# Performance work log

Hardware: AMD Instinct MI355X
Metric: run time of the kernel (lower is better)

The kernel has to match this reference:

```python
import jax, jax.numpy as jnp
import numpy as np
from jax import lax

FH, FW = 5, 5            # kernel_size
DIL_Y, DIL_X = 2, 2      # kernel_dilation
GROUPS = 2               # num_deform_groups
STRIDE_Y, STRIDE_X = 1, 1
PAD_Y, PAD_X = FH // 2, FW // 2
DPAD_Y, DPAD_X = DIL_Y * PAD_Y, DIL_X * PAD_X
OFFSET_NUM = FH * FW * GROUPS * 2  # 100


def setup_inputs() -> dict:
    key = jax.random.key(0)
    k1, k2 = jax.random.split(key, 2)
    B, H, W, C = 2, 192, 384, 16
    volume = jax.random.uniform(k1, (B, H, W, C), dtype=jnp.float32)
    # flax nn.Conv defaults: lecun_normal kernel, zeros bias
    w_off = jax.random.normal(k2, (FH, FW, C, OFFSET_NUM), dtype=jnp.float32) / np.sqrt(FH * FW * C)
    b_off = jnp.zeros((OFFSET_NUM,), dtype=jnp.float32)
    return {"volume": volume, "w_off": w_off, "b_off": b_off}


def _forward(volume, w_off, b_off):
    B, H, W, C = volume.shape
    # offset-predicting conv (VALID, dilated)
    off = lax.conv_general_dilated(
        volume, w_off, (STRIDE_Y, STRIDE_X), 'VALID',
        rhs_dilation=(DIL_Y, DIL_X),
        dimension_numbers=('NHWC', 'HWIO', 'NHWC')) + b_off
    oh, ow = off.shape[1], off.shape[2]
    off = off.reshape(B, oh, ow, FH * FW, 2, GROUPS)
    dy, dx = off[..., 0, :], off[..., 1, :]  # (B,oh,ow,K,G)
    kys = jnp.arange(-DPAD_Y, DPAD_Y + 1, DIL_Y, dtype=jnp.float32)  # (FH,)
    kxs = jnp.arange(-DPAD_X, DPAD_X + 1, DIL_X, dtype=jnp.float32)  # (FW,)
    kv = jnp.repeat(kys, FW)[None, None, None, :, None]  # flat kernel grid, y-offsets
    ku = jnp.tile(kxs, FH)[None, None, None, :, None]    # flat kernel grid, x-offsets
    # Faithful to the source code (including its quirks): rx = kernel_y + dy and
    # ry = kernel_x + dx (names/axes swapped in the original _pixel), the base
    # pixel coordinate is NOT added to the sampling position, and w1 uses the
    # base row index y instead of ry.
    rx = kv + dy
    ry = ku + dx
    x0 = rx.astype(jnp.int32); x1 = x0 + 1  # int32 cast truncates toward zero, as in source
    y0 = ry.astype(jnp.int32); y1 = y0 + 1
    y0 = jnp.clip(y0, 0, H - 1); y1 = jnp.clip(y1, 0, H - 1)
    x0 = jnp.clip(x0, 0, W - 1); x1 = jnp.clip(x1, 0, W - 1)
    by = jnp.arange(DPAD_Y, H - DPAD_Y, STRIDE_Y, dtype=jnp.float32)[None, :, None, None, None]
    w0 = (y1 - ry) * (x1 - rx)
    w1 = (y1 - by) * (rx - x0)
    w2 = (ry - y0) * (x1 - rx)
    w3 = (ry - y0) * (rx - x0)
    # The original sums w_i * p_i over the 4 taps AND all C channels; since the
    # bilinear weights are channel-independent this equals gathering from the
    # channel-summed volume (same math, far fewer gathered bytes).
    S = volume.sum(-1)  # (B,H,W)
    gather = jax.vmap(lambda s, yi, xi: s[yi, xi])  # per-batch fancy gather
    out = (w0 * gather(S, y0, x0) + w1 * gather(S, y0, x1)
           + w2 * gather(S, y1, x0) + w3 * gather(S, y1, x1))  # (B,oh,ow,K,G)
    out = out.reshape(B, oh, ow, FH, FW, GROUPS)
    return jnp.transpose(out, (0, 5, 1, 2, 3, 4))  # (B,G,oh,ow,FH,FW)


def reference(volume, w_off, b_off):
    return _forward(volume, w_off, b_off)
```

## Files before the change

### kernel.cpp

```cpp
#include <hip/hip_runtime.h>

#define HH 192
#define WW 384
#define CC 16
#define OH 184
#define OW 376
#define NTAP 25
#define TILE 64

__global__ void prep_kernel(const float* __restrict__ vol, float* __restrict__ S,
                            const float* __restrict__ w_off, float4* __restrict__ w_t,
                            int nS, int nW) {
    int idx = blockIdx.x * 256 + threadIdx.x;
    if (idx < nS) {
        const float4* p = reinterpret_cast<const float4*>(vol + (size_t)idx * CC);
        float4 a = p[0], b = p[1], c = p[2], d = p[3];
        S[idx] = ((a.x + a.y) + (a.z + a.w)) + ((b.x + b.y) + (b.z + b.w))
               + ((c.x + c.y) + (c.z + c.w)) + ((d.x + d.y) + (d.z + d.w));
    }
    if (idx < nW) {
        int kk = (idx >> 4) % 25;
        int tn = idx / (25 * 16);
        w_t[idx] = *reinterpret_cast<const float4*>(w_off + ((idx & 15) + kk * 16) * 100 + 4 * tn);
    }
}

#define DOT4Q(acc, v, w0, w1, w2, w3) do {                                   \
    acc.x = fmaf(v.x, w0.x, acc.x); acc.x = fmaf(v.y, w1.x, acc.x);          \
    acc.x = fmaf(v.z, w2.x, acc.x); acc.x = fmaf(v.w, w3.x, acc.x);          \
    acc.y = fmaf(v.x, w0.y, acc.y); acc.y = fmaf(v.y, w1.y, acc.y);          \
    acc.y = fmaf(v.z, w2.y, acc.y); acc.y = fmaf(v.w, w3.y, acc.y);          \
    acc.z = fmaf(v.x, w0.z, acc.z); acc.z = fmaf(v.y, w1.z, acc.z);          \
    acc.z = fmaf(v.z, w2.z, acc.z); acc.z = fmaf(v.w, w3.z, acc.z);          \
    acc.w = fmaf(v.x, w0.w, acc.w); acc.w = fmaf(v.y, w1.w, acc.w);          \
    acc.w = fmaf(v.z, w2.w, acc.w); acc.w = fmaf(v.w, w3.w, acc.w);          \
} while (0)

__global__ __launch_bounds__(320) void dconv_kernel(
    const float* __restrict__ vol, const float* __restrict__ w_t,
    const float* __restrict__ b_off, const float* __restrict__ S,
    float* __restrict__ out)
{
    __shared__ float4 lds[4][8][73];

    const int tid  = threadIdx.x;
    const int lane = tid & 63;
    const int wid  = tid >> 6;
    const int z    = blockIdx.z;
    const int kg   = z % 5;
    const int rem  = z / 5;
    const int p    = rem & 1;
    const int b    = rem >> 1;
    const int gy   = blockIdx.y;
    const int ox0  = blockIdx.x * TILE;
    const int tn   = __builtin_amdgcn_readfirstlane(kg * 5 + wid);

    {
        const float* __restrict__ vb = vol + (size_t)((b * HH + p + 8 * gy) * WW) * CC;
        if (tid < 288) {
            const int q    = tid & 3;
            const int colr = tid >> 2;
            int colg = ox0 + colr; if (colg > WW - 1) colg = WW - 1;
            const float* src = vb + (size_t)colg * CC + 4 * q;
            #pragma unroll
            for (int t = 0; t < 8; ++t)
                lds[q][t][colr] = *reinterpret_cast<const float4*>(src + (size_t)(2 * t) * WW * CC);
        }
    }
    __syncthreads();

    const float4* __restrict__ wt = reinterpret_cast<const float4*>(w_t) + tn * (25 * 16);
    const float4 bo = *reinterpret_cast<const float4*>(b_off + 4 * tn);
    float4 acc0 = bo, acc1 = bo, acc2 = bo, acc3 = bo;

    #pragma unroll 1
    for (int r = 0; r < 5; ++r) {
        #pragma unroll
        for (int kx = 0; kx < 5; ++kx) {
            const float4* __restrict__ W = wt + (r * 5 + kx) * 16;
            const int cl = lane + 2 * kx;
            #pragma unroll
            for (int cq = 0; cq < 4; ++cq) {
                const float4 w0 = W[4 * cq + 0], w1 = W[4 * cq + 1];
                const float4 w2 = W[4 * cq + 2], w3 = W[4 * cq + 3];
                const float4 v0 = lds[cq][r + 0][cl];
                const float4 v1 = lds[cq][r + 1][cl];
                const float4 v2 = lds[cq][r + 2][cl];
                const float4 v3 = lds[cq][r + 3][cl];
                DOT4Q(acc0, v0, w0, w1, w2, w3);
                DOT4Q(acc1, v1, w0, w1, w2, w3);
                DOT4Q(acc2, v2, w0, w1, w2, w3);
                DOT4Q(acc3, v3, w0, w1, w2, w3);
            }
        }
    }

    const int ox = ox0 + lane;
    if (ox < OW) {
        const int kyt = tn / 5, kxt = tn % 5;
        const float kv = (float)(2 * kyt - 4);
        const float ku = (float)(2 * kxt - 4);
        const float* __restrict__ Sb = S + b * HH * WW;
        #pragma unroll
        for (int j = 0; j < 4; ++j) {
            const int oy = p + 8 * gy + 2 * j;
            const float4 acc = j == 0 ? acc0 : j == 1 ? acc1 : j == 2 ? acc2 : acc3;
            const float byv = (float)(4 + oy);
            #pragma unroll
            for (int g = 0; g < 2; ++g) {
                const float dy = g == 0 ? acc.x : acc.y;
                const float dx = g == 0 ? acc.z : acc.w;
                const float rx = kv + dy;
                const float ry = ku + dx;
                int x0 = (int)rx;
                int x1 = x0 + 1;
                int y0 = (int)ry;
                int y1 = y0 + 1;
                int x0c = min(max(x0, 0), WW - 1);
                int x1c = min(max(x1, 0), WW - 1);
                int y0c = min(max(y0, 0), HH - 1);
                int y1c = min(max(y1, 0), HH - 1);
                const float fx0 = (float)x0c, fx1 = (float)x1c;
                const float fy0 = (float)y0c, fy1 = (float)y1c;
                const float w0v = (fy1 - ry)  * (fx1 - rx);
                const float w1v = (fy1 - byv) * (rx - fx0);
                const float w2v = (ry - fy0)  * (fx1 - rx);
                const float w3v = (ry - fy0)  * (rx - fx0);
                const float s00 = Sb[y0c * WW + x0c];
                const float s01 = Sb[y0c * WW + x1c];
                const float s10 = Sb[y1c * WW + x0c];
                const float s11 = Sb[y1c * WW + x1c];
                out[(size_t)(((b * 2 + g) * OH + oy) * OW + ox) * NTAP + tn]
                    = w0v * s00 + w1v * s01 + w2v * s10 + w3v * s11;
            }
        }
    }
}

extern "C" void kernel_launch(void* const* d_in, const int* in_sizes, int n_in,
                              void* d_out, int out_size, void* d_ws, size_t ws_size,
                              hipStream_t stream) {
    const float* vol   = (const float*)d_in[0];
    const float* w_off = (const float*)d_in[1];
    const float* b_off = (const float*)d_in[2];
    float* out = (float*)d_out;

    float* S   = (float*)d_ws;
    float* w_t = (float*)((char*)d_ws + 2 * HH * WW * 4);

    const int nS = 2 * HH * WW;
    const int nW = NTAP * 25 * 16;
    prep_kernel<<<(nS + 255) / 256, 256, 0, stream>>>(vol, S, w_off, (float4*)w_t, nS, nW);

    dim3 grid((OW + TILE - 1) / TILE, 23, 2 * 2 * 5);
    dconv_kernel<<<grid, 320, 0, stream>>>(vol, w_t, b_off, S, out);
}
```

Measured before the change: 222.5 us.

## Give each wave five taps over two rows instead of one tap over four rows

The work split changes so that each wave computes 5 output taps (one kernel row) for 2 output rows, instead of 1 tap for 4 rows. The grid drops the tap-group dimension and doubles the row-block dimension. Each block loads 6 input rows instead of 8, and the whole grid reads the input volume once per row block rather than five times, cutting LDS fill and global traffic. In exchange each thread keeps 10 float4 accumulators and reads 5 separate weight streams, which raises register pressure and scalar or vector weight loads.

```diff
diff --git a/kernel.cpp b/kernel.cpp
--- a/kernel.cpp
+++ b/kernel.cpp
@@ -41,97 +41,106 @@
     const float* __restrict__ b_off, const float* __restrict__ S,
     float* __restrict__ out)
 {
-    __shared__ float4 lds[4][8][73];
+    __shared__ float4 lds[4][6][73];
 
     const int tid  = threadIdx.x;
     const int lane = tid & 63;
     const int wid  = tid >> 6;
     const int z    = blockIdx.z;
-    const int kg   = z % 5;
-    const int rem  = z / 5;
-    const int p    = rem & 1;
-    const int b    = rem >> 1;
+    const int p    = z & 1;
+    const int b    = z >> 1;
     const int gy   = blockIdx.y;
+    const int oy0  = p + 4 * gy;
     const int ox0  = blockIdx.x * TILE;
-    const int tn   = __builtin_amdgcn_readfirstlane(kg * 5 + wid);
 
     {
-        const float* __restrict__ vb = vol + (size_t)((b * HH + p + 8 * gy) * WW) * CC;
-        if (tid < 288) {
-            const int q    = tid & 3;
-            const int colr = tid >> 2;
+        const float* __restrict__ vb = vol + (size_t)((b * HH + oy0) * WW) * CC;
+        for (int i = tid; i < 6 * 72 * 4; i += 320) {
+            const int colr = i % 72;
+            const int rem  = i / 72;
+            const int t    = rem % 6;
+            const int q    = rem / 6;
             int colg = ox0 + colr; if (colg > WW - 1) colg = WW - 1;
-            const float* src = vb + (size_t)colg * CC + 4 * q;
-            #pragma unroll
-            for (int t = 0; t < 8; ++t)
-                lds[q][t][colr] = *reinterpret_cast<const float4*>(src + (size_t)(2 * t) * WW * CC);
+            lds[q][t][colr] = *reinterpret_cast<const float4*>(
+                vb + (size_t)(2 * t * WW + colg) * CC + 4 * q);
         }
     }
     __syncthreads();
 
-    const float4* __restrict__ wt = reinterpret_cast<const float4*>(w_t) + tn * (25 * 16);
-    const float4 bo = *reinterpret_cast<const float4*>(b_off + 4 * tn);
-    float4 acc0 = bo, acc1 = bo, acc2 = bo, acc3 = bo;
+    const float4* __restrict__ w4 = reinterpret_cast<const float4*>(w_t);
+    const float4* wtap[5];
+    #pragma unroll
+    for (int tq = 0; tq < 5; ++tq)
+        wtap[tq] = w4 + (size_t)(5 * wid + tq) * 400;
+
+    float4 acc[5][2];
+    #pragma unroll
+    for (int tq = 0; tq < 5; ++tq) {
+        const float4 bo = *reinterpret_cast<const float4*>(b_off + 4 * (5 * wid + tq));
+        acc[tq][0] = bo; acc[tq][1] = bo;
+    }
 
     #pragma unroll 1
     for (int r = 0; r < 5; ++r) {
-        #pragma unroll
+        #pragma unroll 1
         for (int kx = 0; kx < 5; ++kx) {
-            const float4* __restrict__ W = wt + (r * 5 + kx) * 16;
             const int cl = lane + 2 * kx;
+            const int wo = (r * 5 + kx) * 16;
             #pragma unroll
             for (int cq = 0; cq < 4; ++cq) {
-                const float4 w0 = W[4 * cq + 0], w1 = W[4 * cq + 1];
-                const float4 w2 = W[4 * cq + 2], w3 = W[4 * cq + 3];
                 const float4 v0 = lds[cq][r + 0][cl];
                 const float4 v1 = lds[cq][r + 1][cl];
-                const float4 v2 = lds[cq][r + 2][cl];
-                const float4 v3 = lds[cq][r + 3][cl];
-                DOT4Q(acc0, v0, w0, w1, w2, w3);
-                DOT4Q(acc1, v1, w0, w1, w2, w3);
-                DOT4Q(acc2, v2, w0, w1, w2, w3);
-                DOT4Q(acc3, v3, w0, w1, w2, w3);
+                #pragma unroll
+                for (int tq = 0; tq < 5; ++tq) {
+                    const float4* __restrict__ W = wtap[tq] + wo + 4 * cq;
+                    const float4 w0 = W[0], w1 = W[1], w2 = W[2], w3 = W[3];
+                    DOT4Q(acc[tq][0], v0, w0, w1, w2, w3);
+                    DOT4Q(acc[tq][1], v1, w0, w1, w2, w3);
+                }
             }
         }
     }
 
     const int ox = ox0 + lane;
     if (ox < OW) {
-        const int kyt = tn / 5, kxt = tn % 5;
-        const float kv = (float)(2 * kyt - 4);
-        const float ku = (float)(2 * kxt - 4);
         const float* __restrict__ Sb = S + b * HH * WW;
+        const float kv = (float)(2 * wid - 4);
         #pragma unroll
-        for (int j = 0; j < 4; ++j) {
-            const int oy = p + 8 * gy + 2 * j;
-            const float4 acc = j == 0 ? acc0 : j == 1 ? acc1 : j == 2 ? acc2 : acc3;
-            const float byv = (float)(4 + oy);
+        for (int tq = 0; tq < 5; ++tq) {
+            const int tn = 5 * wid + tq;
+            const float ku = (float)(2 * tq - 4);
             #pragma unroll
-            for (int g = 0; g < 2; ++g) {
-                const float dy = g == 0 ? acc.x : acc.y;
-                const float dx = g == 0 ? acc.z : acc.w;
-                const float rx = kv + dy;
-                const float ry = ku + dx;
-                int x0 = (int)rx;
-                int x1 = x0 + 1;
-                int y0 = (int)ry;
-                int y1 = y0 + 1;
-                int x0c = min(max(x0, 0), WW - 1);
-                int x1c = min(max(x1, 0), WW - 1);
-                int y0c = min(max(y0, 0), HH - 1);
-                int y1c = min(max(y1, 0), HH - 1);
-                const float fx0 = (float)x0c, fx1 = (float)x1c;
-                const float fy0 = (float)y0c, fy1 = (float)y1c;
-                const float w0v = (fy1 - ry)  * (fx1 - rx);
-                const float w1v = (fy1 - byv) * (rx - fx0);
-                const float w2v = (ry - fy0)  * (fx1 - rx);
-                const float w3v = (ry - fy0)  * (rx - fx0);
-                const float s00 = Sb[y0c * WW + x0c];
-                const float s01 = Sb[y0c * WW + x1c];
-                const float s10 = Sb[y1c * WW + x0c];
-                const float s11 = Sb[y1c * WW + x1c];
-                out[(size_t)(((b * 2 + g) * OH + oy) * OW + ox) * NTAP + tn]
-                    = w0v * s00 + w1v * s01 + w2v * s10 + w3v * s11;
+            for (int j = 0; j < 2; ++j) {
+                const int oy = oy0 + 2 * j;
+                const float4 a = acc[tq][j];
+                const float byv = (float)(4 + oy);
+                #pragma unroll
+                for (int g = 0; g < 2; ++g) {
+                    const float dy = g == 0 ? a.x : a.y;
+                    const float dx = g == 0 ? a.z : a.w;
+                    const float rx = kv + dy;
+                    const float ry = ku + dx;
+                    int x0 = (int)rx;
+                    int x1 = x0 + 1;
+                    int y0 = (int)ry;
+                    int y1 = y0 + 1;
+                    int x0c = min(max(x0, 0), WW - 1);
+                    int x1c = min(max(x1, 0), WW - 1);
+                    int y0c = min(max(y0, 0), HH - 1);
+                    int y1c = min(max(y1, 0), HH - 1);
+                    const float fx0 = (float)x0c, fx1 = (float)x1c;
+                    const float fy0 = (float)y0c, fy1 = (float)y1c;
+                    const float w0v = (fy1 - ry)  * (fx1 - rx);
+                    const float w1v = (fy1 - byv) * (rx - fx0);
+                    const float w2v = (ry - fy0)  * (fx1 - rx);
+                    const float w3v = (ry - fy0)  * (rx - fx0);
+                    const float s00 = Sb[y0c * WW + x0c];
+                    const float s01 = Sb[y0c * WW + x1c];
+                    const float s10 = Sb[y1c * WW + x0c];
+                    const float s11 = Sb[y1c * WW + x1c];
+                    out[(size_t)(((b * 2 + g) * OH + oy) * OW + ox) * NTAP + tn]
+                        = w0v * s00 + w1v * s01 + w2v * s10 + w3v * s11;
+                }
             }
         }
     }
@@ -152,6 +161,6 @@
     const int nW = NTAP * 25 * 16;
     prep_kernel<<<(nS + 255) / 256, 256, 0, stream>>>(vol, S, w_off, (float4*)w_t, nS, nW);
 
-    dim3 grid((OW + TILE - 1) / TILE, 23, 2 * 2 * 5);
+    dim3 grid((OW + TILE - 1) / TILE, 46, 4);
     dconv_kernel<<<grid, 320, 0, stream>>>(vol, w_t, b_off, S, out);
 }
```

Measured after the change: 493.4 us. 2.22x slower.
